# Optimization experiments

Hardware: AMD Instinct MI355X
Metric: run time of the kernel (lower is better)

## Reference

```python
import jax, jax.numpy as jnp
import numpy as np

EPS = 1e-09


def _glorot(key, shape):
    fan_in, fan_out = shape[-2], shape[-1]
    std = (2.0 / (fan_in + fan_out)) ** 0.5
    return jax.random.normal(key, shape, dtype=jnp.float32) * std


def setup_inputs() -> dict:
    key = jax.random.key(0)
    kx, k1, k2, k3, k4 = jax.random.split(key, 5)
    B, S, D = 2, 1024, 256
    H, K = 8, 32  # key_dim_frac = 1/8
    return {
        "x": jax.random.normal(kx, (B, S, D), dtype=jnp.float32),
        "Wks": _glorot(k1, (H, D, K)),
        "Wqs": _glorot(k2, (H, D, K)),
        "Wvs": _glorot(k3, (H, D, D)),
        "Wo": _glorot(k4, (H, D, D)),
    }


def reference(x, Wks, Wqs, Wvs, Wo):
    # Per-head projections: [H, B, S, K] / [H, B, S, D]
    keys = jnp.einsum('bsd,hdk->hbsk', x, Wks)
    queries = jnp.einsum('bsd,hdk->hbsk', x, Wqs)
    values = jnp.einsum('bsd,hde->hbse', x, Wvs)

    # Feature map: elu + 1 (strictly positive)
    keys = jax.nn.elu(keys) + 1.0
    queries = jax.nn.elu(queries) + 1.0

    # Auxiliary pairwise attention map [H, B, S, S], causal-masked, row-normalized
    att = jnp.einsum('hbsk,hbtk->hbst', queries, keys)
    S = att.shape[-1]
    causal = jnp.tril(jnp.ones((S, S), dtype=att.dtype))
    att = att * causal
    att = att / (jnp.sum(att, axis=-1, keepdims=True) + EPS)

    # Causal linear attention via cumulative sums of outer products
    # [H, B, S, D, K] cumulative state (memory-bound, mirrors tf.cumsum)
    kv = jnp.einsum('hbsk,hbsd->hbsdk', keys, values)
    kv_cum = jnp.cumsum(kv, axis=2)
    numerator = jnp.einsum('hbsdk,hbsk->hbsd', kv_cum, queries)
    denominator = jnp.einsum('hbsk,hbsk->hbs', jnp.cumsum(keys, axis=2), queries)
    node = numerator / (denominator[..., None] + EPS)

    # Output projection, summed over heads: [B, S, D]
    out = jnp.einsum('hbsd,hde->bse', node, Wo)
    return (out, att)
```

## Files before the change

### kernel.cpp

```cpp
#include <hip/hip_runtime.h>
#include <hip/hip_bf16.h>
#include <cstdio>

#define PB 2
#define PS 1024
#define PD 256
#define PK 32
#define PH 8
#define HB (PH*PB)
#define BS (PB*PS)
#define EPS 1e-9f

typedef __attribute__((ext_vector_type(8))) short bf16x8;
typedef __attribute__((ext_vector_type(4))) float f32x4;

__device__ inline unsigned short f2bf(float f) {
    __hip_bfloat16 h = __float2bfloat16(f);
    return *reinterpret_cast<unsigned short*>(&h);
}
__device__ inline float bf2f(unsigned short u) {
    return __bfloat162float(*reinterpret_cast<__hip_bfloat16*>(&u));
}

__global__ __launch_bounds__(256) void k_prep(
    const float* __restrict__ x, const float* __restrict__ Wqs,
    const float* __restrict__ Wks, const float* __restrict__ Wvs,
    const float* __restrict__ Wo,
    unsigned short* __restrict__ xb, unsigned short* __restrict__ WqT,
    unsigned short* __restrict__ WkT, unsigned short* __restrict__ WvT,
    unsigned short* __restrict__ WoT)
{
    __shared__ float smem[8448];
    int bid = blockIdx.x, tid = threadIdx.x;
    if (bid < 512) {
        int i = bid*256 + tid;
        float4 v = ((const float4*)x)[i];
        ushort4 o = {f2bf(v.x), f2bf(v.y), f2bf(v.z), f2bf(v.w)};
        ((ushort4*)xb)[i] = o;
        return;
    }
    if (bid < 528) {
        int r2 = bid - 512;
        int h = r2 >> 1, isK = r2 & 1;
        const float* S = (isK ? Wks : Wqs) + (size_t)h*8192;
        unsigned short* D = (isK ? WkT : WqT) + (size_t)h*8192;
#pragma unroll
        for (int p = 0; p < 32; ++p) {
            int idx = p*256 + tid;
            smem[(idx>>5)*33 + (idx&31)] = S[idx];
        }
        __syncthreads();
#pragma unroll
        for (int p = 0; p < 8; ++p) {
            int o4 = p*256 + tid;
            int kk = o4 >> 6, d = (o4 & 63)*4;
            ushort4 o;
            o.x = f2bf(smem[(d+0)*33 + kk]); o.y = f2bf(smem[(d+1)*33 + kk]);
            o.z = f2bf(smem[(d+2)*33 + kk]); o.w = f2bf(smem[(d+3)*33 + kk]);
            *(ushort4*)(D + (size_t)kk*256 + d) = o;
        }
        return;
    }
    int r3 = bid - 528;
    const float* S; unsigned short* dst; int rs, hs;
    if (r3 < 128) { S = Wvs; dst = WvT; rs = 256;  hs = 65536; }
    else          { r3 -= 128; S = Wo; dst = WoT; rs = 2048; hs = 256; }
    int e0 = (r3 & 3)*64, d0 = ((r3>>2) & 3)*64, h = r3 >> 4;
    float (*T)[69] = (float(*)[69])smem;
    const float* Sh = S + (size_t)h*65536;
    int ty = tid>>4, c4 = tid&15;
#pragma unroll
    for (int p = 0; p < 4; ++p) {
        int r = p*16 + ty;
        float4 v = *(const float4*)(Sh + (size_t)(d0+r)*256 + e0 + c4*4);
        T[r][c4*4+0]=v.x; T[r][c4*4+1]=v.y; T[r][c4*4+2]=v.z; T[r][c4*4+3]=v.w;
    }
    __syncthreads();
    unsigned short* D = dst + (size_t)h*hs;
#pragma unroll
    for (int p = 0; p < 4; ++p) {
        int er = p*16 + ty;
        ushort4 o;
        o.x = f2bf(T[c4*4+0][er]); o.y = f2bf(T[c4*4+1][er]);
        o.z = f2bf(T[c4*4+2][er]); o.w = f2bf(T[c4*4+3][er]);
        *(ushort4*)(D + (size_t)(e0+er)*rs + d0 + c4*4) = o;
    }
}

__global__ __launch_bounds__(256) void k_proj(
    const unsigned short* __restrict__ xb, const unsigned short* __restrict__ WqT,
    const unsigned short* __restrict__ WkT, const unsigned short* __restrict__ WvT,
    unsigned short* __restrict__ Qb, unsigned short* __restrict__ Kb,
    unsigned short* __restrict__ Vt)
{
    int z = blockIdx.z;
    int m0 = blockIdx.y*64, n0 = blockIdx.x*64;
    int tid = threadIdx.x, w = tid>>6, l15 = tid&15, g = (tid>>4)&3;
    f32x4 zf = {0.f,0.f,0.f,0.f};
    f32x4 acc[4] = {zf,zf,zf,zf};
    const unsigned short* arow = xb + (size_t)(m0+16*w+l15)*256 + 8*g;
    const unsigned short* W;
    if (z < 8)       W = WvT + (size_t)z*65536;
    else if (z == 8) W = WqT;
    else             W = WkT;
#pragma unroll
    for (int kk = 0; kk < 8; ++kk) {
        bf16x8 af = *(const bf16x8*)(arow + kk*32);
#pragma unroll
        for (int nt = 0; nt < 4; ++nt) {
            bf16x8 bf = *(const bf16x8*)(W + (size_t)(n0+16*nt+l15)*256 + kk*32 + 8*g);
            acc[nt] = __builtin_amdgcn_mfma_f32_16x16x32_bf16(af, bf, acc[nt], 0, 0, 0);
        }
    }
    if (z < 8) {
        unsigned short* VtT = Vt + ((size_t)z*32 + blockIdx.y)*(256*64);
#pragma unroll
        for (int nt = 0; nt < 4; ++nt) {
            ushort4 o = {f2bf(acc[nt][0]), f2bf(acc[nt][1]), f2bf(acc[nt][2]), f2bf(acc[nt][3])};
            *(ushort4*)(VtT + (size_t)(n0+16*nt+l15)*64 + 16*w + 4*g) = o;
        }
    } else {
        unsigned short* dst = (z == 8) ? Qb : Kb;
        int bs_base = m0 + 16*w + 4*g;
#pragma unroll
        for (int nt = 0; nt < 4; ++nt) {
            int col = n0 + 16*nt + l15;
            int h = col>>5, kk = col&31;
#pragma unroll
            for (int j = 0; j < 4; ++j) {
                int bs = bs_base + j;
                int b = bs>>10, s = bs&1023;
                float zv = acc[nt][j];
                zv = zv > 0.f ? zv + 1.f : expf(zv);
                dst[((size_t)(h*PB+b)*PS + s)*PK + kk] = f2bf(zv);
            }
        }
    }
}

__global__ __launch_bounds__(256) void k_kv_sums(
    const unsigned short* __restrict__ Kb, const unsigned short* __restrict__ Vt,
    float* __restrict__ KVs, float* __restrict__ Ksum)
{
    int c = blockIdx.x, hb = blockIdx.y;
    int tid = threadIdx.x, w = tid>>6, l15 = tid&15, g = (tid>>4)&3;
    __shared__ unsigned short KT[32*72];
    __shared__ float partial[8][32];
#pragma unroll
    for (int i = 0; i < 8; ++i) {
        int flat = tid + i*256;
        KT[(flat&31)*72 + (flat>>5)] = Kb[((size_t)hb*PS + c*64 + (flat>>5))*PK + (flat&31)];
    }
    __syncthreads();
    {
        int kk = tid & 31, part = tid >> 5;
        float s = 0.f;
#pragma unroll
        for (int i = 0; i < 8; ++i) s += bf2f(KT[kk*72 + part*8 + i]);
        partial[part][kk] = s;
    }
    const unsigned short* Vtt = Vt + ((size_t)hb*16 + c)*(256*64);
    f32x4 zf = {0.f,0.f,0.f,0.f};
    f32x4 acc[4][2];
#pragma unroll
    for (int mt = 0; mt < 4; ++mt) { acc[mt][0] = zf; acc[mt][1] = zf; }
#pragma unroll
    for (int ks = 0; ks < 2; ++ks) {
        bf16x8 af[4];
#pragma unroll
        for (int mt = 0; mt < 4; ++mt)
            af[mt] = *(const bf16x8*)(Vtt + (size_t)(64*w + 16*mt + l15)*64 + 32*ks + 8*g);
#pragma unroll
        for (int nt = 0; nt < 2; ++nt) {
            bf16x8 bf = *(const bf16x8*)(KT + (16*nt + l15)*72 + 32*ks + 8*g);
#pragma unroll
            for (int mt = 0; mt < 4; ++mt)
                acc[mt][nt] = __builtin_amdgcn_mfma_f32_16x16x32_bf16(af[mt], bf, acc[mt][nt], 0, 0, 0);
        }
    }
    __syncthreads();
    if (tid < 32) {
        float s = 0.f;
#pragma unroll
        for (int p = 0; p < 8; ++p) s += partial[p][tid];
        Ksum[((size_t)hb*16 + c)*32 + tid] = s;
    }
    float* o = KVs + ((size_t)hb*16 + c)*8192;
#pragma unroll
    for (int mt = 0; mt < 4; ++mt)
#pragma unroll
        for (int nt = 0; nt < 2; ++nt)
#pragma unroll
            for (int j = 0; j < 4; ++j)
                o[(size_t)(64*w + 16*mt + 4*g + j)*32 + 16*nt + l15] = acc[mt][nt][j];
}

__global__ __launch_bounds__(256) void k_mid(
    const float* __restrict__ KVs, const float* __restrict__ Ksum,
    const unsigned short* __restrict__ Qb, const unsigned short* __restrict__ Kb,
    unsigned short* __restrict__ KVpre, float* __restrict__ den)
{
    int hb = blockIdx.y;
    int xb_ = blockIdx.x;
    __shared__ float kc[64][33];
    if (xb_ < 32) {
        int i = xb_*256 + threadIdx.x;
        const float* src = KVs + (size_t)hb*16*8192 + i;
        unsigned short* dst = KVpre + (size_t)hb*16*8192 + i;
        float acc = 0.f;
#pragma unroll
        for (int cc = 0; cc < 16; ++cc) { dst[cc*8192] = f2bf(acc); acc += src[cc*8192]; }
        return;
    }
    int c = xb_ - 32;
    int tid = threadIdx.x;
    int r = tid >> 2, quad = tid & 3;
    bf16x8 k8 = *(const bf16x8*)(Kb + ((size_t)hb*PS + c*64 + r)*PK + quad*8);
#pragma unroll
    for (int i = 0; i < 8; ++i) kc[r][quad*8+i] = bf2f((unsigned short)k8[i]);
    __syncthreads();
#pragma unroll
    for (int st = 1; st < 64; st <<= 1) {
        float tmp[8];
#pragma unroll
        for (int i = 0; i < 8; ++i) tmp[i] = (r >= st) ? kc[r-st][quad*8+i] : 0.f;
        __syncthreads();
#pragma unroll
        for (int i = 0; i < 8; ++i) kc[r][quad*8+i] += tmp[i];
        __syncthreads();
    }
    float kp[8];
#pragma unroll
    for (int i = 0; i < 8; ++i) kp[i] = 0.f;
    for (int cc = 0; cc < c; ++cc) {
        const float* Ks = Ksum + ((size_t)hb*16 + cc)*32 + quad*8;
#pragma unroll
        for (int i = 0; i < 8; ++i) kp[i] += Ks[i];
    }
    bf16x8 q8 = *(const bf16x8*)(Qb + ((size_t)hb*PS + c*64 + r)*PK + quad*8);
    float p = 0.f;
#pragma unroll
    for (int i = 0; i < 8; ++i)
        p += bf2f((unsigned short)q8[i]) * (kp[i] + kc[r][quad*8+i]);
    p += __shfl_xor(p, 1);
    p += __shfl_xor(p, 2);
    if (quad == 0) den[hb*PS + c*64 + r] = p + EPS;
}

__global__ __launch_bounds__(256) void k_att_node(
    const unsigned short* __restrict__ Qb, const unsigned short* __restrict__ Kb,
    const float* __restrict__ den, const unsigned short* __restrict__ Vt,
    const unsigned short* __restrict__ KVpre,
    float* __restrict__ att, unsigned short* __restrict__ nodeB)
{
    int tt = blockIdx.x, st = blockIdx.y, hb = blockIdx.z;
    int s0 = st*64;
    int tid = threadIdx.x, w = tid>>6, l15 = tid&15, g = (tid>>4)&3;
    float* attb = att + (size_t)hb*PS*PS;
    f32x4 zf = {0.f,0.f,0.f,0.f};

    __shared__ __align__(16) unsigned char smem[17664];
    float (*PT)[68] = (float(*)[68])smem;
    unsigned short* PL = (unsigned short*)smem;
    float* rden = (float*)(smem + 17408);

    if (tt < 16) {
        if (tt == st) return;
        if (tt > st) {
            float4 z = {0.f,0.f,0.f,0.f};
            float* base = attb + (size_t)s0*PS + tt*64;
#pragma unroll
            for (int pp = 0; pp < 4; ++pp) {
                int f4 = tid + pp*256;
                int r = f4 >> 4, c4 = f4 & 15;
                *(float4*)(base + (size_t)r*PS + c4*4) = z;
            }
            return;
        }
        if (tid < 64) rden[tid] = 1.0f / den[hb*PS + s0 + tid];
        bf16x8 qf = *(const bf16x8*)(Qb + ((size_t)hb*PS + s0 + 16*w + l15)*PK + 8*g);
        int t0 = tt*64;
        f32x4 p[4];
#pragma unroll
        for (int nt = 0; nt < 4; ++nt) {
            bf16x8 kf = *(const bf16x8*)(Kb + ((size_t)hb*PS + t0 + 16*nt + l15)*PK + 8*g);
            p[nt] = __builtin_amdgcn_mfma_f32_16x16x32_bf16(qf, kf, zf, 0, 0, 0);
        }
        __syncthreads();
        float rd[4];
#pragma unroll
        for (int j = 0; j < 4; ++j) rd[j] = rden[16*w + 4*g + j];
#pragma unroll
        for (int nt = 0; nt < 4; ++nt)
#pragma unroll
            for (int j = 0; j < 4; ++j)
                PT[16*w + 4*g + j][16*nt + l15] = p[nt][j] * rd[j];
        __syncthreads();
#pragma unroll
        for (int pp = 0; pp < 4; ++pp) {
            int f4 = tid + pp*256;
            int r = f4 >> 4, c4 = f4 & 15;
            float4 v = *(const float4*)&PT[r][c4*4];
            *(float4*)(attb + (size_t)(s0+r)*PS + t0 + c4*4) = v;
        }
        return;
    }

    int c = st;
    if (tid < 64) rden[tid] = 1.0f / den[hb*PS + s0 + tid];
    bf16x8 qf = *(const bf16x8*)(Qb + ((size_t)hb*PS + s0 + 16*w + l15)*PK + 8*g);
    const unsigned short* KVp = KVpre + ((size_t)hb*16 + c)*8192;
    f32x4 acc[16];
#pragma unroll
    for (int nt = 0; nt < 16; ++nt) {
        bf16x8 bf = *(const bf16x8*)(KVp + (size_t)(16*nt + l15)*32 + 8*g);
        acc[nt] = __builtin_amdgcn_mfma_f32_16x16x32_bf16(qf, bf, zf, 0, 0, 0);
    }
    f32x4 p[4];
#pragma unroll
    for (int nt4 = 0; nt4 < 4; ++nt4) {
        bf16x8 kf = *(const bf16x8*)(Kb + ((size_t)hb*PS + s0 + 16*nt4 + l15)*PK + 8*g);
        p[nt4] = __builtin_amdgcn_mfma_f32_16x16x32_bf16(qf, kf, zf, 0, 0, 0);
    }
    __syncthreads();
#pragma unroll
    for (int nt4 = 0; nt4 < 4; ++nt4) {
#pragma unroll
        for (int j = 0; j < 4; ++j) {
            int r = 16*w + 4*g + j;
            int tc = 16*nt4 + l15;
            float v = p[nt4][j] * rden[r];
            if (tc > r) v = 0.f;
            attb[(size_t)(s0 + r)*PS + s0 + tc] = v;
            PL[r*72 + tc] = f2bf(v);
        }
    }
#pragma unroll
    for (int nt = 0; nt < 16; ++nt)
#pragma unroll
        for (int j = 0; j < 4; ++j)
            acc[nt][j] *= rden[16*w + 4*g + j];
    __syncthreads();
    const unsigned short* Vtt = Vt + ((size_t)hb*16 + c)*(256*64);
#pragma unroll
    for (int ks = 0; ks < 2; ++ks) {
        bf16x8 af = *(const bf16x8*)(PL + (size_t)(16*w + l15)*72 + 32*ks + 8*g);
#pragma unroll
        for (int nt = 0; nt < 16; ++nt) {
            bf16x8 vf = *(const bf16x8*)(Vtt + (size_t)(16*nt + l15)*64 + 32*ks + 8*g);
            acc[nt] = __builtin_amdgcn_mfma_f32_16x16x32_bf16(af, vf, acc[nt], 0, 0, 0);
        }
    }
    int h = hb >> 1, b = hb & 1;
    unsigned short* np = nodeB + ((size_t)(b*PS + s0))*2048 + h*256;
#pragma unroll
    for (int nt = 0; nt < 16; ++nt)
#pragma unroll
        for (int j = 0; j < 4; ++j)
            np[(size_t)(16*w + 4*g + j)*2048 + 16*nt + l15] = f2bf(acc[nt][j]);
}

__global__ __launch_bounds__(256) void k_out2(
    const unsigned short* __restrict__ nodeB, const unsigned short* __restrict__ WoT,
    float* __restrict__ out)
{
    int e0 = blockIdx.x*64, m0 = blockIdx.y*16;
    int tid = threadIdx.x, w = tid>>6, l15 = tid&15, g = (tid>>4)&3;
    f32x4 zf = {0.f,0.f,0.f,0.f};
    f32x4 acc = zf;
    const unsigned short* arow = nodeB + (size_t)(m0 + l15)*2048 + 8*g;
    const unsigned short* brow = WoT + (size_t)(e0 + 16*w + l15)*2048 + 8*g;
#pragma unroll 8
    for (int kk = 0; kk < 64; ++kk) {
        bf16x8 af = *(const bf16x8*)(arow + kk*32);
        bf16x8 bf = *(const bf16x8*)(brow + kk*32);
        acc = __builtin_amdgcn_mfma_f32_16x16x32_bf16(af, bf, acc, 0, 0, 0);
    }
#pragma unroll
    for (int j = 0; j < 4; ++j)
        out[(size_t)(m0 + 4*g + j)*PD + e0 + 16*w + l15] = acc[j];
}

extern "C" void kernel_launch(void* const* d_in, const int* in_sizes, int n_in,
                              void* d_out, int out_size, void* d_ws, size_t ws_size,
                              hipStream_t stream) {
    const float* x   = (const float*)d_in[0];
    const float* Wks = (const float*)d_in[1];
    const float* Wqs = (const float*)d_in[2];
    const float* Wvs = (const float*)d_in[3];
    const float* Wo  = (const float*)d_in[4];

    float* out = (float*)d_out;
    float* att = (float*)d_out + (size_t)PB*PS*PD;

    float* ws = (float*)d_ws;
    float*          den   = ws + 0;
    unsigned short* Qb    = (unsigned short*)(ws + 16384);
    unsigned short* Kb    = (unsigned short*)(ws + 278528);
    unsigned short* Vt    = (unsigned short*)(ws + 540672);
    unsigned short* xb    = (unsigned short*)(ws + 2637824);
    unsigned short* WqT   = (unsigned short*)(ws + 2899968);
    unsigned short* WkT   = (unsigned short*)(ws + 2932736);
    unsigned short* WvT   = (unsigned short*)(ws + 2965504);
    unsigned short* WoT   = (unsigned short*)(ws + 3227648);
    unsigned short* nodeB = (unsigned short*)(ws + 3489792);
    float*          KVs   = ws + 5586944;
    unsigned short* KVpre = (unsigned short*)(ws + 7684096);
    float*          KsumG = ws + 8732672;
    const size_t needed = (size_t)8740864 * 4;
    if (ws_size < needed) {
        fprintf(stderr, "kernel_launch: ws_size %zu < needed %zu\n", ws_size, needed);
        return;
    }

    k_prep<<<784, 256, 0, stream>>>(x, Wqs, Wks, Wvs, Wo, xb, WqT, WkT, WvT, WoT);
    k_proj<<<dim3(4, 32, 10), 256, 0, stream>>>(xb, WqT, WkT, WvT, Qb, Kb, Vt);
    k_kv_sums<<<dim3(16, HB), 256, 0, stream>>>(Kb, Vt, KVs, KsumG);
    k_mid<<<dim3(48, HB), 256, 0, stream>>>(KVs, KsumG, Qb, Kb, KVpre, den);
    k_att_node<<<dim3(17, 16, HB), 256, 0, stream>>>(Qb, Kb, den, Vt, KVpre, att, nodeB);
    k_out2<<<dim3(4, 128), 256, 0, stream>>>(nodeB, WoT, out);
}
```

Before: 102.3 us.

## Split attention map writer into full-row panel kernel separate from node kernel

Replaces the combined att/node kernel, which wrote 64x64 tiles of the attention map, with a dedicated panel kernel. Each block of that kernel computes 16 full rows (all 1024 columns) in shared memory and writes them as contiguous float4 rows. The node computation moves to its own kernel with 16x16 blocks. The goal is fully coalesced, streaming writes of the large attention output. The cost is an extra launch, 64KB of shared memory per panel block, which limits occupancy, and recomputing the diagonal tiles in both kernels.

```diff
diff --git a/kernel.cpp b/kernel.cpp
--- a/kernel.cpp
+++ b/kernel.cpp
@@ -247,68 +247,67 @@
     if (quad == 0) den[hb*PS + c*64 + r] = p + EPS;
 }
 
-__global__ __launch_bounds__(256) void k_att_node(
+__global__ __launch_bounds__(256) void k_att_panel(
+    const unsigned short* __restrict__ Qb, const unsigned short* __restrict__ Kb,
+    const float* __restrict__ den, float* __restrict__ att)
+{
+    int panel = blockIdx.x, hb = blockIdx.y;
+    int s0 = panel*16;
+    int tid = threadIdx.x, w = tid>>6, l15 = tid&15, g = (tid>>4)&3;
+    __shared__ float P[16*1024];
+    f32x4 zf = {0.f,0.f,0.f,0.f};
+
+    float rd[4];
+#pragma unroll
+    for (int j = 0; j < 4; ++j) rd[j] = 1.0f / den[hb*PS + s0 + 4*g + j];
+
+    bf16x8 qf = *(const bf16x8*)(Qb + ((size_t)hb*PS + s0 + l15)*PK + 8*g);
+
+#pragma unroll
+    for (int i = 0; i < 16; ++i) {
+        int ct = i*4 + w;
+        int t0 = ct*16;
+        int col = t0 + l15;
+        if (t0 > s0 + 15) {
+#pragma unroll
+            for (int j = 0; j < 4; ++j) P[(4*g + j)*1024 + col] = 0.f;
+            continue;
+        }
+        bf16x8 kf = *(const bf16x8*)(Kb + ((size_t)hb*PS + col)*PK + 8*g);
+        f32x4 p = __builtin_amdgcn_mfma_f32_16x16x32_bf16(qf, kf, zf, 0, 0, 0);
+#pragma unroll
+        for (int j = 0; j < 4; ++j) {
+            int r = 4*g + j;
+            float v = p[j] * rd[j];
+            if (col > s0 + r) v = 0.f;
+            P[r*1024 + col] = v;
+        }
+    }
+    __syncthreads();
+    float* dst = att + (size_t)hb*PS*PS + (size_t)s0*PS;
+#pragma unroll
+    for (int i = 0; i < 16; ++i) {
+        float4 v = *(const float4*)&P[i*1024 + tid*4];
+        *(float4*)(dst + (size_t)i*PS + tid*4) = v;
+    }
+}
+
+__global__ __launch_bounds__(256) void k_node(
     const unsigned short* __restrict__ Qb, const unsigned short* __restrict__ Kb,
     const float* __restrict__ den, const unsigned short* __restrict__ Vt,
     const unsigned short* __restrict__ KVpre,
-    float* __restrict__ att, unsigned short* __restrict__ nodeB)
-{
-    int tt = blockIdx.x, st = blockIdx.y, hb = blockIdx.z;
-    int s0 = st*64;
+    unsigned short* __restrict__ nodeB)
+{
+    int c = blockIdx.x, hb = blockIdx.y;
+    int s0 = c*64;
     int tid = threadIdx.x, w = tid>>6, l15 = tid&15, g = (tid>>4)&3;
-    float* attb = att + (size_t)hb*PS*PS;
+    __shared__ unsigned short PL[64*72];
+    __shared__ float rden[64];
+    if (tid < 64) rden[tid] = 1.0f / den[hb*PS + s0 + tid];
+
     f32x4 zf = {0.f,0.f,0.f,0.f};
-
-    __shared__ __align__(16) unsigned char smem[17664];
-    float (*PT)[68] = (float(*)[68])smem;
-    unsigned short* PL = (unsigned short*)smem;
-    float* rden = (float*)(smem + 17408);
-
-    if (tt < 16) {
-        if (tt == st) return;
-        if (tt > st) {
-            float4 z = {0.f,0.f,0.f,0.f};
-            float* base = attb + (size_t)s0*PS + tt*64;
-#pragma unroll
-            for (int pp = 0; pp < 4; ++pp) {
-                int f4 = tid + pp*256;
-                int r = f4 >> 4, c4 = f4 & 15;
-                *(float4*)(base + (size_t)r*PS + c4*4) = z;
-            }
-            return;
-        }
-        if (tid < 64) rden[tid] = 1.0f / den[hb*PS + s0 + tid];
-        bf16x8 qf = *(const bf16x8*)(Qb + ((size_t)hb*PS + s0 + 16*w + l15)*PK + 8*g);
-        int t0 = tt*64;
-        f32x4 p[4];
-#pragma unroll
-        for (int nt = 0; nt < 4; ++nt) {
-            bf16x8 kf = *(const bf16x8*)(Kb + ((size_t)hb*PS + t0 + 16*nt + l15)*PK + 8*g);
-            p[nt] = __builtin_amdgcn_mfma_f32_16x16x32_bf16(qf, kf, zf, 0, 0, 0);
-        }
-        __syncthreads();
-        float rd[4];
-#pragma unroll
-        for (int j = 0; j < 4; ++j) rd[j] = rden[16*w + 4*g + j];
-#pragma unroll
-        for (int nt = 0; nt < 4; ++nt)
-#pragma unroll
-            for (int j = 0; j < 4; ++j)
-                PT[16*w + 4*g + j][16*nt + l15] = p[nt][j] * rd[j];
-        __syncthreads();
-#pragma unroll
-        for (int pp = 0; pp < 4; ++pp) {
-            int f4 = tid + pp*256;
-            int r = f4 >> 4, c4 = f4 & 15;
-            float4 v = *(const float4*)&PT[r][c4*4];
-            *(float4*)(attb + (size_t)(s0+r)*PS + t0 + c4*4) = v;
-        }
-        return;
-    }
-
-    int c = st;
-    if (tid < 64) rden[tid] = 1.0f / den[hb*PS + s0 + tid];
     bf16x8 qf = *(const bf16x8*)(Qb + ((size_t)hb*PS + s0 + 16*w + l15)*PK + 8*g);
+
     const unsigned short* KVp = KVpre + ((size_t)hb*16 + c)*8192;
     f32x4 acc[16];
 #pragma unroll
@@ -331,7 +330,6 @@
             int tc = 16*nt4 + l15;
             float v = p[nt4][j] * rden[r];
             if (tc > r) v = 0.f;
-            attb[(size_t)(s0 + r)*PS + s0 + tc] = v;
             PL[r*72 + tc] = f2bf(v);
         }
     }
@@ -417,6 +415,7 @@
     k_proj<<<dim3(4, 32, 10), 256, 0, stream>>>(xb, WqT, WkT, WvT, Qb, Kb, Vt);
     k_kv_sums<<<dim3(16, HB), 256, 0, stream>>>(Kb, Vt, KVs, KsumG);
     k_mid<<<dim3(48, HB), 256, 0, stream>>>(KVs, KsumG, Qb, Kb, KVpre, den);
-    k_att_node<<<dim3(17, 16, HB), 256, 0, stream>>>(Qb, Kb, den, Vt, KVpre, att, nodeB);
+    k_att_panel<<<dim3(64, HB), 256, 0, stream>>>(Qb, Kb, den, att);
+    k_node<<<dim3(16, HB), 256, 0, stream>>>(Qb, Kb, den, Vt, KVpre, nodeB);
     k_out2<<<dim3(4, 128), 256, 0, stream>>>(nodeB, WoT, out);
 }
```

Measured after the change: 107.3 us. 4.9% more time.
